# Performance work log

Hardware: AMD Instinct MI355X
Metric: run time of the kernel (lower is better)

The kernel has to match this reference:

```python
import jax, jax.numpy as jnp
import numpy as np

TEMP = 0.07
NEG_INF = -1e30  # finite stand-in for -inf; safe under vjp


def setup_inputs() -> dict:
    key = jax.random.key(0)
    k1, k2, k3 = jax.random.split(key, 3)
    B, D, H, F = 16384, 2048, 2048, 128  # 2N rows, backbone_dim, hidden_dim, feature_dim
    features = jax.random.normal(k1, (B, D), dtype=jnp.float32)
    w1 = jax.random.normal(k2, (D, H), dtype=jnp.float32) / np.sqrt(D)
    b1 = jnp.zeros((H,), dtype=jnp.float32)
    w2 = jax.random.normal(k3, (H, F), dtype=jnp.float32) / np.sqrt(H)
    b2 = jnp.zeros((F,), dtype=jnp.float32)
    return {"features": features, "w1": w1, "b1": b1, "w2": w2, "b2": b2}


def reference(features, w1, b1, w2, b2):
    # Projector: Linear -> ReLU -> Linear, then L2-normalize (F.normalize, dim=1)
    h = jax.nn.relu(features @ w1 + b1)
    p = h @ w2 + b2
    z = p / jnp.maximum(jnp.linalg.norm(p, axis=1, keepdims=True), 1e-12)

    M = z.shape[0]           # 2N
    N = M // 2
    sim = (z @ z.T) / TEMP   # [2N, 2N]

    # NT-Xent with labels=0: loss_i = logsumexp_{j != i}(sim[i,j]) - pos_i
    # (pos appears exactly once among the logits, so the gather loop over
    #  per-row negatives collapses to a diagonal-masked row logsumexp).
    diag = jnp.eye(M, dtype=bool)
    lse = jax.nn.logsumexp(jnp.where(diag, NEG_INF, sim), axis=1)
    pos = jnp.sum(z * jnp.roll(z, N, axis=0), axis=1) / TEMP  # sim[i, (i+N) % 2N]
    loss = jnp.mean(lse - pos)
    return loss, z[:N], z[N:]
```

## Files before the change

### kernel.cpp

```cpp
#include <hip/hip_runtime.h>

typedef __attribute__((ext_vector_type(8))) __bf16 bf16x8;
typedef __attribute__((ext_vector_type(4))) float f32x4;

#define B_ROWS 16384
#define N_HALF 8192
#define D_DIM  2048
#define H_DIM  2048
#define F_DIM  128

static constexpr float kInvT = 14.285714285714286f;
static constexpr float kS2   = 20.60992915555662f;

__device__ __forceinline__ void async16(void* lds, const void* g) {
  __builtin_amdgcn_global_load_lds((const __attribute__((address_space(1))) void*)g,
                                   (__attribute__((address_space(3))) void*)lds,
                                   16, 0, 0);
}

__global__ void cvt_bf16_kernel(const float* __restrict__ in, __bf16* __restrict__ out, int n) {
  int i = (blockIdx.x * blockDim.x + threadIdx.x) * 8;
  if (i >= n) return;
  float4 a = *(const float4*)(in + i);
  float4 b = *(const float4*)(in + i + 4);
  bf16x8 o;
  o[0] = (__bf16)a.x; o[1] = (__bf16)a.y; o[2] = (__bf16)a.z; o[3] = (__bf16)a.w;
  o[4] = (__bf16)b.x; o[5] = (__bf16)b.y; o[6] = (__bf16)b.z; o[7] = (__bf16)b.w;
  *(bf16x8*)(out + i) = o;
}

__global__ void transpose_cvt_kernel(const float* __restrict__ in, __bf16* __restrict__ out,
                                     int R, int C) {
  __shared__ float tile[32][33];
  int tx = threadIdx.x, ty = threadIdx.y;
  int c0 = blockIdx.x * 32, r0 = blockIdx.y * 32;
  for (int i = 0; i < 4; i++)
    tile[ty + i * 8][tx] = in[(size_t)(r0 + ty + i * 8) * C + c0 + tx];
  __syncthreads();
  for (int i = 0; i < 4; i++)
    out[(size_t)(c0 + ty + i * 8) * R + r0 + tx] = (__bf16)tile[tx][ty + i * 8];
}

__global__ __launch_bounds__(256) void gemm_relu_kernel(
    const __bf16* __restrict__ A, const __bf16* __restrict__ BT,
    const float* __restrict__ bias, __bf16* __restrict__ C,
    int m_base, int N, int K) {
  __shared__ __align__(16) __bf16 As[128 * 64];
  __shared__ __align__(16) __bf16 Bs[128 * 64];
  const int t = threadIdx.x;
  const int wave = t >> 6, lane = t & 63;
  const int l15 = lane & 15, quad = lane >> 4;
  const int wy = wave >> 1, wx = wave & 1;
  const int m0 = m_base + blockIdx.y * 128, n0 = blockIdx.x * 128;
  const int sr8 = t >> 3;
  const int gk = ((t & 7) ^ (sr8 & 7)) * 8;
  const int l7 = l15 & 7;

  f32x4 acc[4][4];
  for (int i = 0; i < 4; i++)
    for (int j = 0; j < 4; j++) acc[i][j] = 0.f;

  for (int k0 = 0; k0 < K; k0 += 64) {
    for (int q = 0; q < 4; q++)
      async16(As + q * 2048 + wave * 512, A + (size_t)(m0 + q * 32 + sr8) * K + k0 + gk);
    for (int q = 0; q < 4; q++)
      async16(Bs + q * 2048 + wave * 512, BT + (size_t)(n0 + q * 32 + sr8) * K + k0 + gk);
    __syncthreads();
    for (int ks = 0; ks < 2; ks++) {
      bf16x8 af[4], bfr[4];
      const int slot = ((ks * 4 + quad) ^ l7) * 8;
      for (int i = 0; i < 4; i++) {
        af[i]  = *(const bf16x8*)(As + (wy * 64 + i * 16 + l15) * 64 + slot);
        bfr[i] = *(const bf16x8*)(Bs + (wx * 64 + i * 16 + l15) * 64 + slot);
      }
      for (int mi = 0; mi < 4; mi++)
        for (int ni = 0; ni < 4; ni++)
          acc[mi][ni] = __builtin_amdgcn_mfma_f32_16x16x32_bf16(af[mi], bfr[ni], acc[mi][ni], 0, 0, 0);
    }
    __syncthreads();
  }
  for (int ni = 0; ni < 4; ni++) {
    int col = n0 + wx * 64 + ni * 16 + l15;
    float bv = bias[col];
    for (int mi = 0; mi < 4; mi++) {
      int rowb = m0 + wy * 64 + mi * 16 + quad * 4;
      for (int r = 0; r < 4; r++) {
        float v = acc[mi][ni][r] + bv;
        v = fmaxf(v, 0.f);
        C[(size_t)(rowb + r) * N + col] = (__bf16)v;
      }
    }
  }
}

__global__ __launch_bounds__(256) void proj_norm_kernel(
    const __bf16* __restrict__ A, const __bf16* __restrict__ BT,
    const float* __restrict__ bias, float* __restrict__ zf, __bf16* __restrict__ zb, int K) {
  __shared__ __align__(16) __bf16 As[64 * 32];
  __shared__ __align__(16) __bf16 Bs[128 * 32];
  __shared__ float pbuf[64 * 128];
  const int t = threadIdx.x;
  const int wave = t >> 6, lane = t & 63;
  const int l15 = lane & 15, quad = lane >> 4;
  const int wy = wave >> 1, wx = wave & 1;
  const int m0 = blockIdx.x * 64;
  const int sr = t >> 2;
  const int sk = (((t & 3) ^ ((sr >> 1) & 3))) * 8;
  const int sw = (l15 >> 1) & 3;

  f32x4 acc[2][4];
  for (int i = 0; i < 2; i++)
    for (int j = 0; j < 4; j++) acc[i][j] = 0.f;

  for (int k0 = 0; k0 < K; k0 += 32) {
    async16(As + wave * 512, A + (size_t)(m0 + sr) * K + k0 + sk);
    async16(Bs + 0 * 2048 + wave * 512, BT + (size_t)(0  + sr) * K + k0 + sk);
    async16(Bs + 1 * 2048 + wave * 512, BT + (size_t)(64 + sr) * K + k0 + sk);
    __syncthreads();
    bf16x8 af[2], bfr[4];
    for (int i = 0; i < 2; i++)
      af[i] = *(const bf16x8*)(As + (wy * 32 + i * 16 + l15) * 32 + (quad ^ sw) * 8);
    for (int i = 0; i < 4; i++)
      bfr[i] = *(const bf16x8*)(Bs + (wx * 64 + i * 16 + l15) * 32 + (quad ^ sw) * 8);
    for (int mi = 0; mi < 2; mi++)
      for (int ni = 0; ni < 4; ni++)
        acc[mi][ni] = __builtin_amdgcn_mfma_f32_16x16x32_bf16(af[mi], bfr[ni], acc[mi][ni], 0, 0, 0);
    __syncthreads();
  }
  for (int ni = 0; ni < 4; ni++) {
    int col = wx * 64 + ni * 16 + l15;
    float bv = bias[col];
    for (int mi = 0; mi < 2; mi++) {
      int lrow = wy * 32 + mi * 16 + quad * 4;
      for (int r = 0; r < 4; r++)
        pbuf[(lrow + r) * 128 + col] = acc[mi][ni][r] + bv;
    }
  }
  __syncthreads();
  for (int it = 0; it < 16; it++) {
    int lrow = wave * 16 + it;
    float v0 = pbuf[lrow * 128 + lane];
    float v1 = pbuf[lrow * 128 + 64 + lane];
    float ss = v0 * v0 + v1 * v1;
    for (int m = 1; m < 64; m <<= 1) ss += __shfl_xor(ss, m);
    float inv = 1.f / fmaxf(sqrtf(ss), 1e-12f);
    float z0 = v0 * inv, z1 = v1 * inv;
    size_t base = (size_t)(m0 + lrow) * F_DIM;
    zf[base + lane] = z0;
    zf[base + 64 + lane] = z1;
    zb[base + lane] = (__bf16)z0;
    zb[base + 64 + lane] = (__bf16)z1;
  }
}

__global__ __launch_bounds__(256) void sim_lse_kernel(const __bf16* __restrict__ zb,
                                                      float* __restrict__ S) {
  __shared__ __align__(16) __bf16 Bs[128 * 128];
  const int t = threadIdx.x;
  const int wave = t >> 6, lane = t & 63;
  const int l15 = lane & 15, quad = lane >> 4;
  const int wy = wave >> 1, wx = wave & 1;
  const int r0 = blockIdx.y * 128;
  const int c0 = blockIdx.x * 2048;
  const int srow = t >> 4;
  const int schunk = (t & 15) ^ srow;

  bf16x8 a[4][4];
  for (int mi = 0; mi < 4; mi++)
    for (int ks = 0; ks < 4; ks++)
      a[mi][ks] = *(const bf16x8*)(zb + (size_t)(r0 + wy * 64 + mi * 16 + l15) * 128 + ks * 32 + quad * 8);

  float rowacc[4][4];
  for (int mi = 0; mi < 4; mi++)
    for (int r = 0; r < 4; r++) rowacc[mi][r] = 0.f;

  for (int ct = 0; ct < 16; ct++) {
    const __bf16* gbase = zb + (size_t)(c0 + ct * 128) * 128;
    for (int q = 0; q < 8; q++)
      async16(Bs + q * 2048 + wave * 512, gbase + (size_t)(q * 16 + srow) * 128 + schunk * 8);
    __syncthreads();
    const bool diag_tile = (c0 + ct * 128 == r0);
    for (int ni = 0; ni < 4; ni++) {
      bf16x8 b[4];
      const int brow = wx * 64 + ni * 16 + l15;
      for (int ks = 0; ks < 4; ks++)
        b[ks] = *(const bf16x8*)(Bs + brow * 128 + (((ks * 4 + quad) ^ l15) * 8));
      for (int mi = 0; mi < 4; mi++) {
        f32x4 acc = 0.f;
        for (int ks = 0; ks < 4; ks++)
          acc = __builtin_amdgcn_mfma_f32_16x16x32_bf16(a[mi][ks], b[ks], acc, 0, 0, 0);
        if (diag_tile) {
          int j = c0 + ct * 128 + brow;
          int ibase = r0 + wy * 64 + mi * 16 + quad * 4;
          for (int r = 0; r < 4; r++) {
            float term = __builtin_amdgcn_exp2f(fmaf(acc[r], kS2, -kS2));
            rowacc[mi][r] += (ibase + r == j) ? 0.f : term;
          }
        } else {
          for (int r = 0; r < 4; r++)
            rowacc[mi][r] += __builtin_amdgcn_exp2f(fmaf(acc[r], kS2, -kS2));
        }
      }
    }
    __syncthreads();
  }
  for (int mi = 0; mi < 4; mi++)
    for (int r = 0; r < 4; r++) {
      float v = rowacc[mi][r];
      v += __shfl_xor(v, 1);
      v += __shfl_xor(v, 2);
      v += __shfl_xor(v, 4);
      v += __shfl_xor(v, 8);
      if (l15 == 0)
        atomicAdd(&S[r0 + wy * 64 + mi * 16 + quad * 4 + r], v);
    }
}

__global__ void loss_kernel(const float* __restrict__ zf, const float* __restrict__ S,
                            float* __restrict__ out) {
  int wave = threadIdx.x >> 6, lane = threadIdx.x & 63;
  int base = blockIdx.x * 64 + wave * 16;
  float local = 0.f;
  for (int it = 0; it < 16; it++) {
    int row = base + it;
    int j = (row + N_HALF) & (B_ROWS - 1);
    const float* za = zf + (size_t)row * F_DIM;
    const float* zc = zf + (size_t)j * F_DIM;
    float d = za[lane] * zc[lane] + za[lane + 64] * zc[lane + 64];
    for (int m = 1; m < 64; m <<= 1) d += __shfl_xor(d, m);
    float pos = d * kInvT;
    float lse = logf(S[row]) + kInvT;
    local += (lse - pos);
  }
  if (lane == 0) atomicAdd(out, local * (1.f / B_ROWS));
}

extern "C" void kernel_launch(void* const* d_in, const int* in_sizes, int n_in,
                              void* d_out, int out_size, void* d_ws, size_t ws_size,
                              hipStream_t stream) {
  const float* features = (const float*)d_in[0];
  const float* w1 = (const float*)d_in[1];
  const float* b1 = (const float*)d_in[2];
  const float* w2 = (const float*)d_in[3];
  const float* b2 = (const float*)d_in[4];
  float* out = (float*)d_out;

  char* ws = (char*)d_ws;
  size_t off = 0;
  __bf16* A1  = (__bf16*)(ws + off); off += (size_t)B_ROWS * D_DIM * 2;
  __bf16* h   = (__bf16*)(ws + off); off += (size_t)B_ROWS * H_DIM * 2;
  __bf16* w1t = (__bf16*)(ws + off); off += (size_t)H_DIM * D_DIM * 2;
  __bf16* w2t = (__bf16*)(ws + off); off += (size_t)F_DIM * H_DIM * 2;
  __bf16* zbb = (__bf16*)(ws + off); off += (size_t)B_ROWS * F_DIM * 2;
  float*  S   = (float*)(ws + off);  off += (size_t)B_ROWS * 4;

  hipMemsetAsync(S, 0, (size_t)B_ROWS * 4, stream);
  hipMemsetAsync(out, 0, 4, stream);

  {
    int n = B_ROWS * D_DIM;
    cvt_bf16_kernel<<<n / (256 * 8), 256, 0, stream>>>(features, A1, n);
  }
  transpose_cvt_kernel<<<dim3(H_DIM / 32, D_DIM / 32), dim3(32, 8), 0, stream>>>(w1, w1t, D_DIM, H_DIM);
  transpose_cvt_kernel<<<dim3(F_DIM / 32, H_DIM / 32), dim3(32, 8), 0, stream>>>(w2, w2t, H_DIM, F_DIM);

  gemm_relu_kernel<<<dim3(H_DIM / 128, B_ROWS / 256), 256, 0, stream>>>(A1, w1t, b1, h,
                                                                        0, H_DIM, D_DIM);
  gemm_relu_kernel<<<dim3(H_DIM / 128, B_ROWS / 256), 256, 0, stream>>>(A1, w1t, b1, h,
                                                                        B_ROWS / 2, H_DIM, D_DIM);

  proj_norm_kernel<<<B_ROWS / 64, 256, 0, stream>>>(h, w2t, b2, out + 1, zbb, H_DIM);

  sim_lse_kernel<<<dim3(8, B_ROWS / 128), 256, 0, stream>>>(zbb, S);

  loss_kernel<<<B_ROWS / 64, 256, 0, stream>>>(out + 1, S, out);
}
```

Before: 522.1 us.

## Replace first GEMM with 256x256 double-buffered phased MFMA kernel

Swaps the 128x128 single-buffered GEMM1 (launched as two half-grids) for a single-launch 256x256-tile kernel with 512 threads and double-buffered LDS. Each K step is split into four phases with barriers and setprio, so the next tile's async loads overlap MFMA work. The block index is remapped so blocks that run together share tiles in cache. The intent is to hide global-load latency and raise data reuse per tile, at the cost of more LDS (128KB) and more registers per block, which limits occupancy.

```diff
diff --git a/kernel.cpp b/kernel.cpp
--- a/kernel.cpp
+++ b/kernel.cpp
@@ -41,53 +41,149 @@
     out[(size_t)(c0 + ty + i * 8) * R + r0 + tx] = (__bf16)tile[tx][ty + i * 8];
 }
 
-__global__ __launch_bounds__(256) void gemm_relu_kernel(
+#define BM 256
+#define BK 64
+#define NT_K (D_DIM / BK)
+
+__global__ __launch_bounds__(512, 2) void gemm1_8ph_kernel(
     const __bf16* __restrict__ A, const __bf16* __restrict__ BT,
-    const float* __restrict__ bias, __bf16* __restrict__ C,
-    int m_base, int N, int K) {
-  __shared__ __align__(16) __bf16 As[128 * 64];
-  __shared__ __align__(16) __bf16 Bs[128 * 64];
+    const float* __restrict__ bias, __bf16* __restrict__ C) {
+  __shared__ __align__(16) __bf16 As[2][BM * BK];
+  __shared__ __align__(16) __bf16 Bs[2][BM * BK];
   const int t = threadIdx.x;
   const int wave = t >> 6, lane = t & 63;
-  const int l15 = lane & 15, quad = lane >> 4;
-  const int wy = wave >> 1, wx = wave & 1;
-  const int m0 = m_base + blockIdx.y * 128, n0 = blockIdx.x * 128;
-  const int sr8 = t >> 3;
-  const int gk = ((t & 7) ^ (sr8 & 7)) * 8;
-  const int l7 = l15 & 7;
-
-  f32x4 acc[4][4];
-  for (int i = 0; i < 4; i++)
-    for (int j = 0; j < 4; j++) acc[i][j] = 0.f;
-
-  for (int k0 = 0; k0 < K; k0 += 64) {
-    for (int q = 0; q < 4; q++)
-      async16(As + q * 2048 + wave * 512, A + (size_t)(m0 + q * 32 + sr8) * K + k0 + gk);
-    for (int q = 0; q < 4; q++)
-      async16(Bs + q * 2048 + wave * 512, BT + (size_t)(n0 + q * 32 + sr8) * K + k0 + gk);
-    __syncthreads();
-    for (int ks = 0; ks < 2; ks++) {
-      bf16x8 af[4], bfr[4];
-      const int slot = ((ks * 4 + quad) ^ l7) * 8;
-      for (int i = 0; i < 4; i++) {
-        af[i]  = *(const bf16x8*)(As + (wy * 64 + i * 16 + l15) * 64 + slot);
-        bfr[i] = *(const bf16x8*)(Bs + (wx * 64 + i * 16 + l15) * 64 + slot);
-      }
-      for (int mi = 0; mi < 4; mi++)
-        for (int ni = 0; ni < 4; ni++)
-          acc[mi][ni] = __builtin_amdgcn_mfma_f32_16x16x32_bf16(af[mi], bfr[ni], acc[mi][ni], 0, 0, 0);
-    }
-    __syncthreads();
-  }
-  for (int ni = 0; ni < 4; ni++) {
-    int col = n0 + wx * 64 + ni * 16 + l15;
+  const int l15 = lane & 15, quad = lane >> 4, l7 = l15 & 7;
+  const int wy = wave & 1, wx = wave >> 1;
+
+  const int wg = ((int)blockIdx.x & 7) * 64 + ((int)blockIdx.x >> 3);
+  const int n0 = (wg & 7) * 256;
+  const int m0 = (wg >> 3) * 256;
+
+  const int tr = t >> 3;
+  const int csw = ((t & 7) ^ (tr & 7)) * 8;
+  const __bf16* pA = A + (size_t)(m0 + tr) * D_DIM + csw;
+  const __bf16* pB = BT + (size_t)(n0 + tr) * D_DIM + csw;
+  const int ldsw = wave * 512;
+
+  auto stageA = [&](int buf, int h, int kk) {
+    async16(&As[buf][h * 8192 + ldsw], pA + (size_t)(h * 128) * D_DIM + kk);
+    async16(&As[buf][h * 8192 + 4096 + ldsw], pA + (size_t)(h * 128 + 64) * D_DIM + kk);
+  };
+  auto stageB = [&](int buf, int h, int kk) {
+    async16(&Bs[buf][h * 8192 + ldsw], pB + (size_t)(h * 128) * D_DIM + kk);
+    async16(&Bs[buf][h * 8192 + 4096 + ldsw], pB + (size_t)(h * 128 + 64) * D_DIM + kk);
+  };
+
+  const int arow = wy * 16 + l15;
+  const int brow = wx * 16 + l15;
+  const int s0 = (quad ^ l7) * 8;
+  const int s1 = ((4 + quad) ^ l7) * 8;
+
+  f32x4 acc[8][4];
+#pragma unroll
+  for (int f = 0; f < 8; f++)
+#pragma unroll
+    for (int n = 0; n < 4; n++) acc[f][n] = 0.f;
+
+  stageB(0, 0, 0); stageB(0, 1, 0);
+  stageA(0, 0, 0); stageA(0, 1, 0);
+  stageB(1, 0, BK); stageB(1, 1, BK);
+  asm volatile("s_waitcnt vmcnt(4)" ::: "memory");
+  __builtin_amdgcn_s_barrier();
+
+  for (int tk = 0; tk < NT_K; ++tk) {
+    const int cur = tk & 1, nxt = cur ^ 1;
+    const __bf16* Ac = &As[cur][0];
+    const __bf16* Bc = &Bs[cur][0];
+#define LDA(f, s) (*(const bf16x8*)(Ac + ((f) * 32 + arow) * 64 + (s)))
+#define LDB(n, s) (*(const bf16x8*)(Bc + ((n) * 64 + brow) * 64 + (s)))
+    bf16x8 b0[4], b1[4];
+    {
+      bf16x8 a0 = LDA(0, s0), a1 = LDA(1, s0), a2 = LDA(2, s0), a3 = LDA(3, s0);
+      b0[0] = LDB(0, s0); b0[1] = LDB(1, s0); b0[2] = LDB(2, s0); b0[3] = LDB(3, s0);
+      if (tk + 1 < NT_K) stageA(nxt, 0, (tk + 1) * BK);
+      __builtin_amdgcn_s_barrier();
+      asm volatile("s_waitcnt lgkmcnt(0)" ::: "memory");
+      __builtin_amdgcn_s_setprio(1);
+#pragma unroll
+      for (int n = 0; n < 4; n++) {
+        acc[0][n] = __builtin_amdgcn_mfma_f32_16x16x32_bf16(a0, b0[n], acc[0][n], 0, 0, 0);
+        acc[1][n] = __builtin_amdgcn_mfma_f32_16x16x32_bf16(a1, b0[n], acc[1][n], 0, 0, 0);
+        acc[2][n] = __builtin_amdgcn_mfma_f32_16x16x32_bf16(a2, b0[n], acc[2][n], 0, 0, 0);
+        acc[3][n] = __builtin_amdgcn_mfma_f32_16x16x32_bf16(a3, b0[n], acc[3][n], 0, 0, 0);
+      }
+      __builtin_amdgcn_s_setprio(0);
+      __builtin_amdgcn_s_barrier();
+    }
+    {
+      bf16x8 a4 = LDA(4, s0), a5 = LDA(5, s0), a6 = LDA(6, s0), a7 = LDA(7, s0);
+      if (tk + 1 < NT_K) stageA(nxt, 1, (tk + 1) * BK);
+      __builtin_amdgcn_s_barrier();
+      asm volatile("s_waitcnt lgkmcnt(0)" ::: "memory");
+      __builtin_amdgcn_s_setprio(1);
+#pragma unroll
+      for (int n = 0; n < 4; n++) {
+        acc[4][n] = __builtin_amdgcn_mfma_f32_16x16x32_bf16(a4, b0[n], acc[4][n], 0, 0, 0);
+        acc[5][n] = __builtin_amdgcn_mfma_f32_16x16x32_bf16(a5, b0[n], acc[5][n], 0, 0, 0);
+        acc[6][n] = __builtin_amdgcn_mfma_f32_16x16x32_bf16(a6, b0[n], acc[6][n], 0, 0, 0);
+        acc[7][n] = __builtin_amdgcn_mfma_f32_16x16x32_bf16(a7, b0[n], acc[7][n], 0, 0, 0);
+      }
+      __builtin_amdgcn_s_setprio(0);
+      __builtin_amdgcn_s_barrier();
+    }
+    {
+      bf16x8 a0 = LDA(0, s1), a1 = LDA(1, s1), a2 = LDA(2, s1), a3 = LDA(3, s1);
+      b1[0] = LDB(0, s1); b1[1] = LDB(1, s1); b1[2] = LDB(2, s1); b1[3] = LDB(3, s1);
+      __builtin_amdgcn_s_barrier();
+      asm volatile("s_waitcnt lgkmcnt(0)" ::: "memory");
+      __builtin_amdgcn_s_setprio(1);
+#pragma unroll
+      for (int n = 0; n < 4; n++) {
+        acc[0][n] = __builtin_amdgcn_mfma_f32_16x16x32_bf16(a0, b1[n], acc[0][n], 0, 0, 0);
+        acc[1][n] = __builtin_amdgcn_mfma_f32_16x16x32_bf16(a1, b1[n], acc[1][n], 0, 0, 0);
+        acc[2][n] = __builtin_amdgcn_mfma_f32_16x16x32_bf16(a2, b1[n], acc[2][n], 0, 0, 0);
+        acc[3][n] = __builtin_amdgcn_mfma_f32_16x16x32_bf16(a3, b1[n], acc[3][n], 0, 0, 0);
+      }
+      __builtin_amdgcn_s_setprio(0);
+      __builtin_amdgcn_s_barrier();
+    }
+    {
+      bf16x8 a4 = LDA(4, s1), a5 = LDA(5, s1), a6 = LDA(6, s1), a7 = LDA(7, s1);
+      if (tk + 2 < NT_K) {
+        stageB(cur, 0, (tk + 2) * BK);
+        stageB(cur, 1, (tk + 2) * BK);
+        asm volatile("s_waitcnt vmcnt(4)" ::: "memory");
+      } else if (tk + 1 < NT_K) {
+        asm volatile("s_waitcnt vmcnt(0)" ::: "memory");
+      }
+      __builtin_amdgcn_s_barrier();
+      asm volatile("s_waitcnt lgkmcnt(0)" ::: "memory");
+      __builtin_amdgcn_s_setprio(1);
+#pragma unroll
+      for (int n = 0; n < 4; n++) {
+        acc[4][n] = __builtin_amdgcn_mfma_f32_16x16x32_bf16(a4, b1[n], acc[4][n], 0, 0, 0);
+        acc[5][n] = __builtin_amdgcn_mfma_f32_16x16x32_bf16(a5, b1[n], acc[5][n], 0, 0, 0);
+        acc[6][n] = __builtin_amdgcn_mfma_f32_16x16x32_bf16(a6, b1[n], acc[6][n], 0, 0, 0);
+        acc[7][n] = __builtin_amdgcn_mfma_f32_16x16x32_bf16(a7, b1[n], acc[7][n], 0, 0, 0);
+      }
+      __builtin_amdgcn_s_setprio(0);
+      __builtin_amdgcn_s_barrier();
+    }
+#undef LDA
+#undef LDB
+  }
+
+#pragma unroll
+  for (int n = 0; n < 4; n++) {
+    int col = n0 + n * 64 + wx * 16 + l15;
     float bv = bias[col];
-    for (int mi = 0; mi < 4; mi++) {
-      int rowb = m0 + wy * 64 + mi * 16 + quad * 4;
+#pragma unroll
+    for (int f = 0; f < 8; f++) {
+      int rowb = m0 + f * 32 + wy * 16 + quad * 4;
+#pragma unroll
       for (int r = 0; r < 4; r++) {
-        float v = acc[mi][ni][r] + bv;
-        v = fmaxf(v, 0.f);
-        C[(size_t)(rowb + r) * N + col] = (__bf16)v;
+        float v = fmaxf(acc[f][n][r] + bv, 0.f);
+        C[(size_t)(rowb + r) * H_DIM + col] = (__bf16)v;
       }
     }
   }
@@ -264,10 +360,7 @@
   transpose_cvt_kernel<<<dim3(H_DIM / 32, D_DIM / 32), dim3(32, 8), 0, stream>>>(w1, w1t, D_DIM, H_DIM);
   transpose_cvt_kernel<<<dim3(F_DIM / 32, H_DIM / 32), dim3(32, 8), 0, stream>>>(w2, w2t, H_DIM, F_DIM);
 
-  gemm_relu_kernel<<<dim3(H_DIM / 128, B_ROWS / 256), 256, 0, stream>>>(A1, w1t, b1, h,
-                                                                        0, H_DIM, D_DIM);
-  gemm_relu_kernel<<<dim3(H_DIM / 128, B_ROWS / 256), 256, 0, stream>>>(A1, w1t, b1, h,
-                                                                        B_ROWS / 2, H_DIM, D_DIM);
+  gemm1_8ph_kernel<<<dim3((B_ROWS / 256) * (H_DIM / 256)), 512, 0, stream>>>(A1, w1t, b1, h);
 
   proj_norm_kernel<<<B_ROWS / 64, 256, 0, stream>>>(h, w2t, b2, out + 1, zbb, H_DIM);
 
```

Result: faster. 487.3 us (-6.7%).
